# Optimization experiments

Hardware: AMD Instinct MI355X
Metric: run time of the kernel (lower is better)

## Reference

```python
import jax, jax.numpy as jnp
import numpy as np

N_NODES = 10000
N_EDGES = 200000
NODE_DIM = 128
EDGE_DIM = 16
CONV_DIM = 64
HEADS = 5
NEG_SLOPE = 0.2


def gatv2_layer(x, src, dst, edge_attr, Wl, bl, We, att, bias):
    # PyG GATv2Conv, share_weights=True, concat=False, add_self_loops=True, eval mode
    N = x.shape[0]
    H, C = att.shape
    xl = (x @ Wl + bl).reshape(N, H, C)  # [N,H,C]; x_r = x_l (share_weights)
    # self loops, edge_attr fill_value='mean' (mean of incoming edge_attr per node)
    deg = jax.ops.segment_sum(jnp.ones(dst.shape[0], x.dtype), dst, num_segments=N)
    loop_attr = jax.ops.segment_sum(edge_attr, dst, num_segments=N) / jnp.maximum(deg, 1.0)[:, None]
    loop = jnp.arange(N, dtype=src.dtype)
    src_f = jnp.concatenate([src, loop])
    dst_f = jnp.concatenate([dst, loop])
    ea = jnp.concatenate([edge_attr, loop_attr], axis=0)
    e_emb = (ea @ We).reshape(-1, H, C)  # [E+N,H,C]
    m = jax.nn.leaky_relu(xl[src_f] + xl[dst_f] + e_emb, NEG_SLOPE)
    score = jnp.einsum('ehc,hc->eh', m, att)  # [E+N,H]
    # per-destination softmax over incoming edges
    smax = jax.ops.segment_max(score, dst_f, num_segments=N)
    ex = jnp.exp(score - smax[dst_f])
    denom = jax.ops.segment_sum(ex, dst_f, num_segments=N)
    alpha = ex / denom[dst_f]
    out = jax.ops.segment_sum(alpha[:, :, None] * xl[src_f], dst_f, num_segments=N)
    return out.mean(axis=1) + bias  # concat=False -> mean over heads


def setup_inputs() -> dict:
    key = jax.random.key(0)
    ks = jax.random.split(key, 32)
    inp = {
        'x': jax.random.normal(ks[0], (N_NODES, NODE_DIM), jnp.float32),
        'edge_index': jax.random.randint(ks[1], (2, N_EDGES), 0, N_NODES, dtype=jnp.int32),
        'edge_attr': jax.random.normal(ks[2], (N_EDGES, EDGE_DIM), jnp.float32),
    }
    in_dims = [NODE_DIM, CONV_DIM, CONV_DIM]
    HC = HEADS * CONV_DIM
    k = 3
    for l in range(3):
        d = in_dims[l]
        inp[f'Wl{l}'] = jax.random.normal(ks[k], (d, HC), jnp.float32) / np.float32(np.sqrt(d)); k += 1
        inp[f'bl{l}'] = jnp.zeros((HC,), jnp.float32)
        inp[f'We{l}'] = jax.random.normal(ks[k], (EDGE_DIM, HC), jnp.float32) / np.float32(np.sqrt(EDGE_DIM)); k += 1
        inp[f'att{l}'] = jax.random.normal(ks[k], (HEADS, CONV_DIM), jnp.float32) / np.float32(np.sqrt(CONV_DIM)); k += 1
        inp[f'b{l}'] = jnp.zeros((CONV_DIM,), jnp.float32)
    return inp


def reference(x, edge_index, edge_attr,
              Wl0, bl0, We0, att0, b0,
              Wl1, bl1, We1, att1, b1,
              Wl2, bl2, We2, att2, b2):
    src, dst = edge_index[0], edge_index[1]
    h = x
    layers = [(Wl0, bl0, We0, att0, b0), (Wl1, bl1, We1, att1, b1), (Wl2, bl2, We2, att2, b2)]
    for Wl, bl, We, att, b in layers:
        h = gatv2_layer(h, src, dst, edge_attr, Wl, bl, We, att, b)
        h = jax.nn.elu(h)
    return h
```

## Files before the change

kernel.cpp:

```cpp
#include <hip/hip_runtime.h>
#include <hip/hip_bf16.h>


#define NN 10000
#define NE 200000
#define ND 128
#define ED 16
#define CD 64
#define NH 5
#define HC 320
#define EF 210000
#define EFP 210048
#define NEG 0.2f
#define WPH 1641
#define TOT2 8205
#define G2 8208

typedef float f2 __attribute__((ext_vector_type(2)));

__global__ void k_count(const int* __restrict__ dst, int* __restrict__ deg) {
  int e = blockIdx.x * blockDim.x + threadIdx.x;
  if (e >= NE) return;
  atomicAdd(&deg[dst[e]], 1);
}

__global__ __launch_bounds__(1024) void k_scan(const int* __restrict__ deg,
                                               int* __restrict__ rowptr) {
  __shared__ int part[1024];
  int t = threadIdx.x;
  int base = t * 10;
  int local[10];
  int s = 0;
  #pragma unroll
  for (int j = 0; j < 10; j++) {
    int i = base + j;
    local[j] = (i < NN) ? deg[i] : 0;
    s += local[j];
  }
  part[t] = s;
  __syncthreads();
  for (int off = 1; off < 1024; off <<= 1) {
    int v = (t >= off) ? part[t - off] : 0;
    __syncthreads();
    part[t] += v;
    __syncthreads();
  }
  int prefix = (t > 0) ? part[t - 1] : 0;
  #pragma unroll
  for (int j = 0; j < 10; j++) {
    int i = base + j;
    if (i < NN) rowptr[i] = prefix;
    prefix += local[j];
  }
  if (t == 1023) rowptr[NN] = prefix;
}

__global__ void k_fill(const int* __restrict__ ei, const int* __restrict__ rowptr,
                       int* __restrict__ cursor, int* __restrict__ csr_eid,
                       int* __restrict__ srcx, int* __restrict__ dstx) {
  int e = blockIdx.x * blockDim.x + threadIdx.x;
  if (e >= NE) return;
  int d = ei[NE + e];
  int slot = atomicAdd(&cursor[d], 1);
  int pos = rowptr[d] + slot;
  csr_eid[pos] = e;
  srcx[pos] = ei[e];
  dstx[pos] = d;
}

__global__ void k_selfext(int* __restrict__ srcx, int* __restrict__ dstx) {
  int i = blockIdx.x * blockDim.x + threadIdx.x;
  int p = NE + i;
  if (p >= EFP) return;
  int v = (p < EF) ? (p - NE) : 0;
  srcx[p] = v;
  dstx[p] = v;
}

__global__ __launch_bounds__(256) void k_loopattr(const int* __restrict__ csr_eid,
                                                  const int* __restrict__ rowptr,
                                                  const float* __restrict__ eattr,
                                                  float* __restrict__ loop_attr) {
  int wave = threadIdx.x >> 6, lane = threadIdx.x & 63;
  int d = blockIdx.x * 4 + wave;
  if (d >= NN) return;
  int g = lane >> 4, k = lane & 15;
  int b = rowptr[d], n = rowptr[d + 1] - b;
  float s = 0.f;
  for (int i = g; i < n; i += 4)
    s += eattr[(size_t)csr_eid[b + i] * ED + k];
  s += __shfl_xor(s, 16, 64);
  s += __shfl_xor(s, 32, 64);
  if (g == 0) loop_attr[d * ED + k] = s / fmaxf((float)n, 1.0f);
}

__global__ void k_ea2(const int* __restrict__ csr_eid, const float* __restrict__ eattr,
                      const float* __restrict__ loop_attr, float* __restrict__ ea2) {
  int idx = blockIdx.x * blockDim.x + threadIdx.x;
  if (idx >= EFP * ED) return;
  int p = idx >> 4, k = idx & 15;
  float v;
  if (p < NE)      v = eattr[(size_t)csr_eid[p] * ED + k];
  else if (p < EF) v = loop_attr[(size_t)(p - NE) * ED + k];
  else             v = 0.f;
  ea2[((size_t)(p >> 1) * 32) + 2 * k + (p & 1)] = v;
}

template <int D>
__global__ __launch_bounds__(320) void k_xl(const float* __restrict__ h,
                                            const float* __restrict__ Wl,
                                            const float* __restrict__ bl,
                                            float* __restrict__ xl) {
  constexpr int NPB = 8;
  int node0 = blockIdx.x * NPB;
  int t = threadIdx.x;
  float acc[NPB];
  #pragma unroll
  for (int i = 0; i < NPB; i++) acc[i] = 0.f;
  for (int k = 0; k < D; k += 4) {
    float w0 = Wl[(k + 0) * HC + t];
    float w1 = Wl[(k + 1) * HC + t];
    float w2 = Wl[(k + 2) * HC + t];
    float w3 = Wl[(k + 3) * HC + t];
    #pragma unroll
    for (int i = 0; i < NPB; i++) {
      float4 hv = *(const float4*)(h + (size_t)(node0 + i) * D + k);
      acc[i] += hv.x * w0 + hv.y * w1 + hv.z * w2 + hv.w * w3;
    }
  }
  float bv = bl[t];
  int hh = t >> 6, c = t & 63;
  #pragma unroll
  for (int i = 0; i < NPB; i++)
    xl[((size_t)hh * NN + node0 + i) * CD + c] = acc[i] + bv;
}

__global__ __launch_bounds__(256) void k_score(
    const int* __restrict__ srcx, const int* __restrict__ dstx,
    const float* __restrict__ ea2, const float* __restrict__ xl,
    const float* __restrict__ We, const float* __restrict__ att,
    float* __restrict__ wP) {
  __shared__ float lds[4][64][34];
  int wk = (blockIdx.x & 7) * 1026 + (blockIdx.x >> 3);
  if (wk >= TOT2) return;
  int h  = wk / WPH;
  int lb = wk - h * WPH;
  int wave = __builtin_amdgcn_readfirstlane(threadIdx.x >> 6);
  int lane = threadIdx.x & 63;
  int p0 = lb * 128 + wave * 32;

  f2 wv[16];
  #pragma unroll
  for (int k = 0; k < 16; k++) {
    float w = We[k * HC + h * CD + lane];
    wv[k] = f2{w, w};
  }
  float a1 = att[h * CD + lane];
  f2 av = f2{a1, a1};
  const float* xh = xl + (size_t)h * NN * CD;
  const f2 zero = {0.f, 0.f};

  f2 acc[16];
  #pragma unroll
  for (int i = 0; i < 16; i++) {
    int p = p0 + 2 * i;
    int s0 = srcx[p], s1 = srcx[p + 1];
    int d0 = dstx[p], d1 = dstx[p + 1];
    const f2* e = (const f2*)(ea2 + (size_t)(p >> 1) * 32);
    float xs0 = xh[(size_t)s0 * CD + lane];
    float xs1 = xh[(size_t)s1 * CD + lane];
    float xd0 = xh[(size_t)d0 * CD + lane];
    float xd1 = xh[(size_t)d1 * CD + lane];
    f2 z = f2{xs0 + xd0, xs1 + xd1};
    #pragma unroll
    for (int k = 0; k < 16; k++)
      z += e[k] * wv[k];
    z = __builtin_elementwise_max(z, zero) + NEG * __builtin_elementwise_min(z, zero);
    acc[i] = z * av;
  }

  float (*L)[34] = lds[wave];
  #pragma unroll
  for (int i = 0; i < 16; i++)
    *(f2*)&L[lane][2 * i] = acc[i];
  int part = lane >> 5, j = lane & 31;
  float sum = 0.f;
  #pragma unroll
  for (int r = 0; r < 32; r++)
    sum += L[part * 32 + r][j];
  sum += __shfl_xor(sum, 32, 64);
  if (part == 0) {
    float sc = fminf(fmaxf(sum, -60.f), 60.f);
    wP[(size_t)h * EFP + p0 + j] = __expf(sc);
  }
}

__global__ __launch_bounds__(320) void k_agg(
    const int* __restrict__ csr_src, const int* __restrict__ rowptr,
    const float* __restrict__ wP, const float* __restrict__ xl,
    const float* __restrict__ bias, float* __restrict__ out) {
  __shared__ float s_v[NH][CD];
  int h = threadIdx.x >> 6, lane = threadIdx.x & 63;
  int d = blockIdx.x;
  int b = rowptr[d], n = rowptr[d + 1] - b;
  const float* sp = wP + (size_t)h * EFP;
  const float* xlh = xl + (size_t)h * NN * CD + lane;
  float dn = sp[NE + d];
  float acc = dn * xlh[(size_t)d * CD];
  int p = b, pe = b + n;
  for (; p + 4 <= pe; p += 4) {
    int s0 = csr_src[p], s1 = csr_src[p + 1], s2 = csr_src[p + 2], s3 = csr_src[p + 3];
    float w0 = sp[p], w1 = sp[p + 1], w2 = sp[p + 2], w3 = sp[p + 3];
    float x0 = xlh[(size_t)s0 * CD];
    float x1 = xlh[(size_t)s1 * CD];
    float x2 = xlh[(size_t)s2 * CD];
    float x3 = xlh[(size_t)s3 * CD];
    dn += (w0 + w1) + (w2 + w3);
    acc += w0 * x0 + w1 * x1 + w2 * x2 + w3 * x3;
  }
  for (; p < pe; p++) {
    int s0 = csr_src[p];
    float w0 = sp[p];
    dn += w0;
    acc += w0 * xlh[(size_t)s0 * CD];
  }
  s_v[h][lane] = acc / dn;
  __syncthreads();
  if (h == 0) {
    float v = s_v[0][lane] + s_v[1][lane] + s_v[2][lane] + s_v[3][lane] + s_v[4][lane];
    v = v * (1.0f / NH) + bias[lane];
    v = v > 0.f ? v : expm1f(v);
    out[(size_t)d * CD + lane] = v;
  }
}

static inline size_t aln(size_t x) { return (x + 255) & ~(size_t)255; }

extern "C" void kernel_launch(void* const* d_in, const int* in_sizes, int n_in,
                              void* d_out, int out_size, void* d_ws, size_t ws_size,
                              hipStream_t stream) {
  const float* x = (const float*)d_in[0];
  const int* ei = (const int*)d_in[1];
  const float* eattr = (const float*)d_in[2];

  char* w = (char*)d_ws;
  int* degi      = (int*)w;                 w += aln(NN * 4);
  int* cursor    = (int*)w;                 w += aln(NN * 4);
  int* rowptr    = (int*)w;                 w += aln((NN + 1) * 4);
  int* csr_eid   = (int*)w;                 w += aln((size_t)NE * 4);
  int* srcx      = (int*)w;                 w += aln((size_t)EFP * 4);
  int* dstx      = (int*)w;                 w += aln((size_t)EFP * 4);
  float* loop_attr = (float*)w;             w += aln((size_t)NN * ED * 4);
  float* ea2     = (float*)w;               w += aln((size_t)EFP * ED * 4);
  float* xl      = (float*)w;               w += aln((size_t)NN * HC * 4);
  float* wPbuf   = (float*)w;               w += aln((size_t)NH * EFP * 4);
  float* hbuf    = (float*)w;               w += aln((size_t)NN * CD * 4);

  hipMemsetAsync(degi, 0, NN * 4, stream);
  hipMemsetAsync(cursor, 0, NN * 4, stream);
  k_count<<<(NE + 255) / 256, 256, 0, stream>>>(ei + NE, degi);
  k_scan<<<1, 1024, 0, stream>>>(degi, rowptr);
  k_fill<<<(NE + 255) / 256, 256, 0, stream>>>(ei, rowptr, cursor, csr_eid, srcx, dstx);
  k_selfext<<<(EFP - NE + 255) / 256, 256, 0, stream>>>(srcx, dstx);
  k_loopattr<<<(NN + 3) / 4, 256, 0, stream>>>(csr_eid, rowptr, eattr, loop_attr);
  k_ea2<<<(EFP * ED + 255) / 256, 256, 0, stream>>>(csr_eid, eattr, loop_attr, ea2);

  for (int l = 0; l < 3; l++) {
    const float* Wl  = (const float*)d_in[3 + 5 * l];
    const float* bl  = (const float*)d_in[4 + 5 * l];
    const float* We  = (const float*)d_in[5 + 5 * l];
    const float* att = (const float*)d_in[6 + 5 * l];
    const float* b   = (const float*)d_in[7 + 5 * l];

    if (l == 0) k_xl<ND><<<NN / 8, 320, 0, stream>>>(x, Wl, bl, xl);
    else        k_xl<CD><<<NN / 8, 320, 0, stream>>>(hbuf, Wl, bl, xl);

    k_score<<<G2, 256, 0, stream>>>(srcx, dstx, ea2, xl, We, att, wPbuf);

    float* dst_out = (l < 2) ? hbuf : (float*)d_out;
    k_agg<<<NN, 320, 0, stream>>>(srcx, rowptr, wPbuf, xl, b, dst_out);
  }
}
```

Measured before the change: 532.5 us.

## Fuse attention scoring and aggregation into one per-destination kernel

Replaces the separate edge-score kernel and aggregation kernel with a single per-destination-node kernel. Each head's wave walks the node's CSR edges in pairs, computes the GATv2 logits with a wave-wide shuffle reduction, exponentiates them and accumulates the softmax numerator and denominator in the same pass. The self-loop term is computed inline from `loop_attr`, which is now derived from the reordered `ea2` buffer. `xl` moves to a node-major [N, H*C] layout. This removes the `wP` buffer round trip, the destination gathers and several setup kernels, at the cost of serial per-edge shuffle reductions and a longer dependent loop per block.

```diff
diff --git a/kernel.cpp b/kernel.cpp
--- a/kernel.cpp
+++ b/kernel.cpp
@@ -9,12 +9,7 @@
 #define CD 64
 #define NH 5
 #define HC 320
-#define EF 210000
-#define EFP 210048
 #define NEG 0.2f
-#define WPH 1641
-#define TOT2 8205
-#define G2 8208
 
 typedef float f2 __attribute__((ext_vector_type(2)));
 
@@ -57,29 +52,27 @@
 
 __global__ void k_fill(const int* __restrict__ ei, const int* __restrict__ rowptr,
                        int* __restrict__ cursor, int* __restrict__ csr_eid,
-                       int* __restrict__ srcx, int* __restrict__ dstx) {
+                       int* __restrict__ csr_src) {
   int e = blockIdx.x * blockDim.x + threadIdx.x;
   if (e >= NE) return;
   int d = ei[NE + e];
   int slot = atomicAdd(&cursor[d], 1);
   int pos = rowptr[d] + slot;
   csr_eid[pos] = e;
-  srcx[pos] = ei[e];
-  dstx[pos] = d;
-}
-
-__global__ void k_selfext(int* __restrict__ srcx, int* __restrict__ dstx) {
-  int i = blockIdx.x * blockDim.x + threadIdx.x;
-  int p = NE + i;
-  if (p >= EFP) return;
-  int v = (p < EF) ? (p - NE) : 0;
-  srcx[p] = v;
-  dstx[p] = v;
-}
-
-__global__ __launch_bounds__(256) void k_loopattr(const int* __restrict__ csr_eid,
+  csr_src[pos] = ei[e];
+}
+
+__global__ void k_ea2(const int* __restrict__ csr_eid, const float* __restrict__ eattr,
+                      float* __restrict__ ea2) {
+  int idx = blockIdx.x * blockDim.x + threadIdx.x;
+  if (idx >= NE * ED) return;
+  int p = idx >> 4, k = idx & 15;
+  float v = eattr[(size_t)csr_eid[p] * ED + k];
+  ea2[((size_t)(p >> 1) * 32) + 2 * k + (p & 1)] = v;
+}
+
+__global__ __launch_bounds__(256) void k_loopattr(const float* __restrict__ ea2,
                                                   const int* __restrict__ rowptr,
-                                                  const float* __restrict__ eattr,
                                                   float* __restrict__ loop_attr) {
   int wave = threadIdx.x >> 6, lane = threadIdx.x & 63;
   int d = blockIdx.x * 4 + wave;
@@ -87,23 +80,13 @@
   int g = lane >> 4, k = lane & 15;
   int b = rowptr[d], n = rowptr[d + 1] - b;
   float s = 0.f;
-  for (int i = g; i < n; i += 4)
-    s += eattr[(size_t)csr_eid[b + i] * ED + k];
+  for (int i = g; i < n; i += 4) {
+    int p = b + i;
+    s += ea2[((size_t)(p >> 1) * 32) + 2 * k + (p & 1)];
+  }
   s += __shfl_xor(s, 16, 64);
   s += __shfl_xor(s, 32, 64);
   if (g == 0) loop_attr[d * ED + k] = s / fmaxf((float)n, 1.0f);
-}
-
-__global__ void k_ea2(const int* __restrict__ csr_eid, const float* __restrict__ eattr,
-                      const float* __restrict__ loop_attr, float* __restrict__ ea2) {
-  int idx = blockIdx.x * blockDim.x + threadIdx.x;
-  if (idx >= EFP * ED) return;
-  int p = idx >> 4, k = idx & 15;
-  float v;
-  if (p < NE)      v = eattr[(size_t)csr_eid[p] * ED + k];
-  else if (p < EF) v = loop_attr[(size_t)(p - NE) * ED + k];
-  else             v = 0.f;
-  ea2[((size_t)(p >> 1) * 32) + 2 * k + (p & 1)] = v;
 }
 
 template <int D>
@@ -129,101 +112,73 @@
     }
   }
   float bv = bl[t];
-  int hh = t >> 6, c = t & 63;
   #pragma unroll
   for (int i = 0; i < NPB; i++)
-    xl[((size_t)hh * NN + node0 + i) * CD + c] = acc[i] + bv;
-}
-
-__global__ __launch_bounds__(256) void k_score(
-    const int* __restrict__ srcx, const int* __restrict__ dstx,
-    const float* __restrict__ ea2, const float* __restrict__ xl,
-    const float* __restrict__ We, const float* __restrict__ att,
-    float* __restrict__ wP) {
-  __shared__ float lds[4][64][34];
-  int wk = (blockIdx.x & 7) * 1026 + (blockIdx.x >> 3);
-  if (wk >= TOT2) return;
-  int h  = wk / WPH;
-  int lb = wk - h * WPH;
-  int wave = __builtin_amdgcn_readfirstlane(threadIdx.x >> 6);
-  int lane = threadIdx.x & 63;
-  int p0 = lb * 128 + wave * 32;
-
-  f2 wv[16];
-  #pragma unroll
-  for (int k = 0; k < 16; k++) {
-    float w = We[k * HC + h * CD + lane];
-    wv[k] = f2{w, w};
-  }
-  float a1 = att[h * CD + lane];
-  f2 av = f2{a1, a1};
-  const float* xh = xl + (size_t)h * NN * CD;
+    xl[(size_t)(node0 + i) * HC + t] = acc[i] + bv;
+}
+
+__global__ __launch_bounds__(320) void k_fused(
+    const int* __restrict__ csr_src, const int* __restrict__ rowptr,
+    const float* __restrict__ ea2, const float* __restrict__ loop_attr,
+    const float* __restrict__ xl, const float* __restrict__ We,
+    const float* __restrict__ att, const float* __restrict__ bias,
+    float* __restrict__ out) {
+  __shared__ float s_v[NH][CD];
+  int bid = blockIdx.x;
+  int d = (bid & 7) * (NN / 8) + (bid >> 3);
+  int h = threadIdx.x >> 6, lane = threadIdx.x & 63;
+  int b = rowptr[d];
+  int pe = rowptr[d + 1];
+  float wv[16];
+  #pragma unroll
+  for (int k = 0; k < 16; k++) wv[k] = We[k * HC + h * CD + lane];
+  float a = att[h * CD + lane];
+  const float* xrow = xl + h * CD + lane;
+  float xd = xrow[(size_t)d * HC];
   const f2 zero = {0.f, 0.f};
 
-  f2 acc[16];
-  #pragma unroll
-  for (int i = 0; i < 16; i++) {
-    int p = p0 + 2 * i;
-    int s0 = srcx[p], s1 = srcx[p + 1];
-    int d0 = dstx[p], d1 = dstx[p + 1];
-    const f2* e = (const f2*)(ea2 + (size_t)(p >> 1) * 32);
-    float xs0 = xh[(size_t)s0 * CD + lane];
-    float xs1 = xh[(size_t)s1 * CD + lane];
-    float xd0 = xh[(size_t)d0 * CD + lane];
-    float xd1 = xh[(size_t)d1 * CD + lane];
-    f2 z = f2{xs0 + xd0, xs1 + xd1};
+  float dn, acc;
+  {
+    const float* la = loop_attr + (size_t)d * ED;
+    float z = xd + xd;
+    #pragma unroll
+    for (int k = 0; k < 16; k++) z += la[k] * wv[k];
+    z = fmaxf(z, 0.f) + NEG * fminf(z, 0.f);
+    float sc = z * a;
+    #pragma unroll
+    for (int off = 1; off < 64; off <<= 1) sc += __shfl_xor(sc, off, 64);
+    sc = fminf(fmaxf(sc, -60.f), 60.f);
+    float w = __expf(sc);
+    dn = w;
+    acc = w * xd;
+  }
+
+  int tb = b >> 1, te = (pe + 1) >> 1;
+  for (int t = tb; t < te; t++) {
+    int p0 = 2 * t, p1 = 2 * t + 1;
+    int s0 = csr_src[p0], s1 = csr_src[p1];
+    const f2* e2 = (const f2*)(ea2 + (size_t)t * 32);
+    float xs0 = xrow[(size_t)s0 * HC];
+    float xs1 = xrow[(size_t)s1 * HC];
+    f2 z = f2{xs0 + xd, xs1 + xd};
     #pragma unroll
     for (int k = 0; k < 16; k++)
-      z += e[k] * wv[k];
+      z += e2[k] * f2{wv[k], wv[k]};
     z = __builtin_elementwise_max(z, zero) + NEG * __builtin_elementwise_min(z, zero);
-    acc[i] = z * av;
-  }
-
-  float (*L)[34] = lds[wave];
-  #pragma unroll
-  for (int i = 0; i < 16; i++)
-    *(f2*)&L[lane][2 * i] = acc[i];
-  int part = lane >> 5, j = lane & 31;
-  float sum = 0.f;
-  #pragma unroll
-  for (int r = 0; r < 32; r++)
-    sum += L[part * 32 + r][j];
-  sum += __shfl_xor(sum, 32, 64);
-  if (part == 0) {
-    float sc = fminf(fmaxf(sum, -60.f), 60.f);
-    wP[(size_t)h * EFP + p0 + j] = __expf(sc);
-  }
-}
-
-__global__ __launch_bounds__(320) void k_agg(
-    const int* __restrict__ csr_src, const int* __restrict__ rowptr,
-    const float* __restrict__ wP, const float* __restrict__ xl,
-    const float* __restrict__ bias, float* __restrict__ out) {
-  __shared__ float s_v[NH][CD];
-  int h = threadIdx.x >> 6, lane = threadIdx.x & 63;
-  int d = blockIdx.x;
-  int b = rowptr[d], n = rowptr[d + 1] - b;
-  const float* sp = wP + (size_t)h * EFP;
-  const float* xlh = xl + (size_t)h * NN * CD + lane;
-  float dn = sp[NE + d];
-  float acc = dn * xlh[(size_t)d * CD];
-  int p = b, pe = b + n;
-  for (; p + 4 <= pe; p += 4) {
-    int s0 = csr_src[p], s1 = csr_src[p + 1], s2 = csr_src[p + 2], s3 = csr_src[p + 3];
-    float w0 = sp[p], w1 = sp[p + 1], w2 = sp[p + 2], w3 = sp[p + 3];
-    float x0 = xlh[(size_t)s0 * CD];
-    float x1 = xlh[(size_t)s1 * CD];
-    float x2 = xlh[(size_t)s2 * CD];
-    float x3 = xlh[(size_t)s3 * CD];
-    dn += (w0 + w1) + (w2 + w3);
-    acc += w0 * x0 + w1 * x1 + w2 * x2 + w3 * x3;
-  }
-  for (; p < pe; p++) {
-    int s0 = csr_src[p];
-    float w0 = sp[p];
-    dn += w0;
-    acc += w0 * xlh[(size_t)s0 * CD];
-  }
+    f2 sc = z * f2{a, a};
+    #pragma unroll
+    for (int off = 1; off < 64; off <<= 1) {
+      sc.x += __shfl_xor(sc.x, off, 64);
+      sc.y += __shfl_xor(sc.y, off, 64);
+    }
+    sc = __builtin_elementwise_min(__builtin_elementwise_max(sc, f2{-60.f, -60.f}),
+                                   f2{60.f, 60.f});
+    float w0 = (p0 >= b) ? __expf(sc.x) : 0.f;
+    float w1 = (p1 < pe) ? __expf(sc.y) : 0.f;
+    dn += w0 + w1;
+    acc += w0 * xs0 + w1 * xs1;
+  }
+
   s_v[h][lane] = acc / dn;
   __syncthreads();
   if (h == 0) {
@@ -248,22 +203,19 @@
   int* cursor    = (int*)w;                 w += aln(NN * 4);
   int* rowptr    = (int*)w;                 w += aln((NN + 1) * 4);
   int* csr_eid   = (int*)w;                 w += aln((size_t)NE * 4);
-  int* srcx      = (int*)w;                 w += aln((size_t)EFP * 4);
-  int* dstx      = (int*)w;                 w += aln((size_t)EFP * 4);
+  int* csr_src   = (int*)w;                 w += aln((size_t)NE * 4);
   float* loop_attr = (float*)w;             w += aln((size_t)NN * ED * 4);
-  float* ea2     = (float*)w;               w += aln((size_t)EFP * ED * 4);
+  float* ea2     = (float*)w;               w += aln((size_t)NE * ED * 4);
   float* xl      = (float*)w;               w += aln((size_t)NN * HC * 4);
-  float* wPbuf   = (float*)w;               w += aln((size_t)NH * EFP * 4);
   float* hbuf    = (float*)w;               w += aln((size_t)NN * CD * 4);
 
   hipMemsetAsync(degi, 0, NN * 4, stream);
   hipMemsetAsync(cursor, 0, NN * 4, stream);
   k_count<<<(NE + 255) / 256, 256, 0, stream>>>(ei + NE, degi);
   k_scan<<<1, 1024, 0, stream>>>(degi, rowptr);
-  k_fill<<<(NE + 255) / 256, 256, 0, stream>>>(ei, rowptr, cursor, csr_eid, srcx, dstx);
-  k_selfext<<<(EFP - NE + 255) / 256, 256, 0, stream>>>(srcx, dstx);
-  k_loopattr<<<(NN + 3) / 4, 256, 0, stream>>>(csr_eid, rowptr, eattr, loop_attr);
-  k_ea2<<<(EFP * ED + 255) / 256, 256, 0, stream>>>(csr_eid, eattr, loop_attr, ea2);
+  k_fill<<<(NE + 255) / 256, 256, 0, stream>>>(ei, rowptr, cursor, csr_eid, csr_src);
+  k_ea2<<<(NE * ED + 255) / 256, 256, 0, stream>>>(csr_eid, eattr, ea2);
+  k_loopattr<<<(NN + 3) / 4, 256, 0, stream>>>(ea2, rowptr, loop_attr);
 
   for (int l = 0; l < 3; l++) {
     const float* Wl  = (const float*)d_in[3 + 5 * l];
@@ -275,9 +227,8 @@
     if (l == 0) k_xl<ND><<<NN / 8, 320, 0, stream>>>(x, Wl, bl, xl);
     else        k_xl<CD><<<NN / 8, 320, 0, stream>>>(hbuf, Wl, bl, xl);
 
-    k_score<<<G2, 256, 0, stream>>>(srcx, dstx, ea2, xl, We, att, wPbuf);
-
     float* dst_out = (l < 2) ? hbuf : (float*)d_out;
-    k_agg<<<NN, 320, 0, stream>>>(srcx, rowptr, wPbuf, xl, b, dst_out);
-  }
-}
+    k_fused<<<NN, 320, 0, stream>>>(csr_src, rowptr, ea2, loop_attr,
+                                    xl, We, att, b, dst_out);
+  }
+}
```

New measurement: 508.7 us. 4.5% less time.
